# Kernel tuning notes

Measured on AMD Instinct MI355X. Metric: run time of the kernel, lower is better.

## Reference

```python
import jax, jax.numpy as jnp
import numpy as np

B, N1, N2 = 4, 16384, 4096   # scenes, fine points/scene, coarse points/scene
CIN, COUT = 512, 256
K = 3
EPS_BN = 1e-5
EPS_D = 1e-8


def setup_inputs() -> dict:
    key = jax.random.key(0)
    ks = jax.random.split(key, 6)
    return {
        "point_1": jax.random.uniform(ks[0], (B * N1, 3), dtype=jnp.float32),
        "feat_1": jax.random.normal(ks[1], (B * N1, COUT), dtype=jnp.float32) * 0.1,
        "point_2": jax.random.uniform(ks[2], (B * N2, 3), dtype=jnp.float32),
        "feat_2": jax.random.normal(ks[3], (B * N2, CIN), dtype=jnp.float32) * 0.1,
        "W1": jax.random.normal(ks[4], (COUT, COUT), dtype=jnp.float32) / np.sqrt(COUT).astype(np.float32),
        "b1": jnp.zeros((COUT,), jnp.float32),
        "g1": jnp.ones((COUT,), jnp.float32),
        "beta1": jnp.zeros((COUT,), jnp.float32),
        "W2": jax.random.normal(ks[5], (CIN, COUT), dtype=jnp.float32) / np.sqrt(CIN).astype(np.float32),
        "b2": jnp.zeros((COUT,), jnp.float32),
        "g2": jnp.ones((COUT,), jnp.float32),
        "beta2": jnp.zeros((COUT,), jnp.float32),
        # equal-sized segments: row_splits = [0, N, 2N, ...]
        "row_splits_1": jnp.arange(B + 1, dtype=jnp.int32) * N1,
        "row_splits_2": jnp.arange(B + 1, dtype=jnp.int32) * N2,
    }


def _bn(x, gamma, beta):
    # BatchNorm1d, training mode (biased variance, as in torch)
    mu = x.mean(0)
    var = x.var(0)
    return gamma * (x - mu) * jax.lax.rsqrt(var + EPS_BN) + beta


def reference(point_1, feat_1, point_2, feat_2,
              W1, b1, g1, beta1, W2, b2, g2, beta2,
              row_splits_1, row_splits_2):
    # linear1(feat_1): Linear + BN + ReLU
    f1 = jax.nn.relu(_bn(feat_1 @ W1 + b1, g1, beta1))          # [B*N1, COUT]
    # linear2(feat_2): Linear + BN + ReLU
    f2 = jax.nn.relu(_bn(feat_2 @ W2 + b2, g2, beta2))          # [B*N2, COUT]

    # batched KNN (equal row_splits -> reshape into [B, n, 3])
    q = point_1.reshape(B, N1, 3)
    p = point_2.reshape(B, N2, 3)
    d2 = ((q * q).sum(-1)[:, :, None]
          + (p * p).sum(-1)[:, None, :]
          - 2.0 * jnp.einsum("bnd,bmd->bnm", q, p))             # [B, N1, N2] squared dists
    neg_d, idx = jax.lax.top_k(-d2, K)                           # [B, N1, K]
    dist = jnp.maximum(-neg_d, 0.0)

    # inverse-distance weights (knn search is non-differentiable in the original)
    recip = 1.0 / (dist + EPS_D)
    w = jax.lax.stop_gradient(recip / recip.sum(-1, keepdims=True))  # [B, N1, K]

    # gather + weighted sum (three-interpolate)
    f2b = f2.reshape(B, N2, COUT)
    gathered = f2b[jnp.arange(B)[:, None, None], idx]            # [B, N1, K, COUT]
    interp = (gathered * w[..., None]).sum(2).reshape(B * N1, COUT)

    return f1 + interp
```

## Files before the change

### kernel.cpp

```cpp
#include <hip/hip_runtime.h>
#include <hip/hip_bf16.h>
#include <math.h>

#define N1R 65536
#define N2R 16384
#define NPB 4096
#define NQB 16384
#define CC  256
#define ASTRIDE 40
#define NCELL 512
#define GRID_FAIL_R2 0.015625f

typedef __attribute__((ext_vector_type(4))) float v4f;
typedef __attribute__((ext_vector_type(8))) short v8s;

static __device__ __forceinline__ short f2bs(float f) {
    union { __hip_bfloat16 h; short s; } u;
    u.h = __float2bfloat16(f);
    return u.s;
}

static __device__ __forceinline__ int cell_of(float x, float y, float z) {
    const int cx = min(7, (int)(x * 8.0f));
    const int cy = min(7, (int)(y * 8.0f));
    const int cz = min(7, (int)(z * 8.0f));
    return (cz << 6) | (cy << 3) | cx;
}

static __device__ __forceinline__ void ins3(float d, int si,
    float& b0, float& b1, float& b2, int& i0, int& i1, int& i2)
{
    const bool lt0 = (d < b0) | ((d == b0) & (si < i0));
    const bool lt1 = (d < b1) | ((d == b1) & (si < i1));
    const bool lt2 = (d < b2) | ((d == b2) & (si < i2));
    b2 = lt1 ? b1 : (lt2 ? d : b2);   i2 = lt1 ? i1 : (lt2 ? si : i2);
    b1 = lt0 ? b0 : (lt1 ? d : b1);   i1 = lt0 ? i0 : (lt1 ? si : i1);
    b0 = lt0 ? d  : b0;               i0 = lt0 ? si : i0;
}

__global__ __launch_bounds__(256)
void wtrans_kernel(const float* __restrict__ W, short* __restrict__ WT, int Kd)
{
    const int i = blockIdx.x * 256 + threadIdx.x;
    const int k = i >> 8;
    const int n = i & 255;
    WT[(size_t)n * Kd + k] = f2bs(W[i]);
}

__global__ __launch_bounds__(256)
void paug_count_kernel(const float* __restrict__ p2, float4* __restrict__ paug,
                       int* __restrict__ counts_p)
{
#pragma clang fp contract(off)
    const int i = blockIdx.x * 256 + threadIdx.x;
    const float x = p2[(size_t)i * 3 + 0];
    const float y = p2[(size_t)i * 3 + 1];
    const float z = p2[(size_t)i * 3 + 2];
    float4 v;
    v.x = x; v.y = y; v.z = z;
    v.w = (x * x + y * y) + z * z;
    paug[i] = v;
    const int b = i >> 12;
    atomicAdd(&counts_p[b * NCELL + cell_of(x, y, z)], 1);
}

__global__ __launch_bounds__(256)
void qcount_kernel(const float* __restrict__ p1, int* __restrict__ counts_q)
{
    const int i = blockIdx.x * 256 + threadIdx.x;
    const float x = p1[(size_t)i * 3 + 0];
    const float y = p1[(size_t)i * 3 + 1];
    const float z = p1[(size_t)i * 3 + 2];
    const int b = i >> 14;
    atomicAdd(&counts_q[b * NCELL + cell_of(x, y, z)], 1);
}

__global__ __launch_bounds__(512)
void prefix_kernel(const int* __restrict__ counts_p, int* __restrict__ cursors_p,
                   int* __restrict__ starts_p,
                   const int* __restrict__ counts_q, int* __restrict__ cursors_q)
{
    __shared__ int sc[512];
    const int t = threadIdx.x;
    for (int a = 0; a < 8; ++a) {
        const int b = a & 3;
        const int* cnt = (a < 4) ? counts_p + b * NCELL : counts_q + b * NCELL;
        const int v = cnt[t];
        sc[t] = v;
        __syncthreads();
        for (int off = 1; off < 512; off <<= 1) {
            const int add = (t >= off) ? sc[t - off] : 0;
            __syncthreads();
            sc[t] += add;
            __syncthreads();
        }
        const int incl = sc[t];
        const int excl = incl - v;
        if (a < 4) {
            starts_p[b * 513 + t] = excl;
            if (t == 511) starts_p[b * 513 + 512] = incl;
            cursors_p[b * NCELL + t] = excl;
        } else {
            cursors_q[b * NCELL + t] = excl;
        }
        __syncthreads();
    }
}

__global__ __launch_bounds__(256)
void scatter_p_kernel(const float4* __restrict__ paug, int* __restrict__ cursors,
                      float4* __restrict__ sortedP, unsigned short* __restrict__ sIdx)
{
    const int i = blockIdx.x * 256 + threadIdx.x;
    const float4 v = paug[i];
    const int b = i >> 12;
    const int cell = cell_of(v.x, v.y, v.z);
    const int pos = atomicAdd(&cursors[b * NCELL + cell], 1);
    sortedP[(size_t)b * NPB + pos] = v;
    sIdx[(size_t)b * NPB + pos] = (unsigned short)(i & 4095);
}

__global__ __launch_bounds__(256)
void scatter_q_kernel(const float* __restrict__ p1, int* __restrict__ cursors,
                      unsigned short* __restrict__ qlist)
{
    const int i = blockIdx.x * 256 + threadIdx.x;
    const float x = p1[(size_t)i * 3 + 0];
    const float y = p1[(size_t)i * 3 + 1];
    const float z = p1[(size_t)i * 3 + 2];
    const int b = i >> 14;
    const int cell = cell_of(x, y, z);
    const int pos = atomicAdd(&cursors[b * NCELL + cell], 1);
    qlist[(size_t)b * NQB + pos] = (unsigned short)(i & 16383);
}

__global__ __launch_bounds__(256)
void gemm_fused_kernel(const float* __restrict__ X,
                       const short* __restrict__ WT,
                       const float* __restrict__ bias,
                       float* __restrict__ Y,
                       float* __restrict__ partS, float* __restrict__ partQ,
                       int Kdim)
{
    __shared__ short As[128 * ASTRIDE];

    const int bm0 = blockIdx.x * 128;
    const int bn0 = blockIdx.y * 128;
    const int wave = threadIdx.x >> 6;
    const int lane = threadIdx.x & 63;
    const int wm0 = (wave >> 1) * 64;
    const int wn0 = (wave & 1) * 64;
    const int col = lane & 15, quad = lane >> 4;

    const int srow = threadIdx.x >> 1;
    const int skh  = (threadIdx.x & 1) * 16;
    const float* sbase = X + (size_t)(bm0 + srow) * Kdim + skh;
    short* sdst = As + srow * ASTRIDE + skh;

    v4f acc[4][4];
#pragma unroll
    for (int i = 0; i < 4; ++i)
#pragma unroll
        for (int j = 0; j < 4; ++j) acc[i][j] = (v4f){0.f, 0.f, 0.f, 0.f};

    const short* wbase = WT + (size_t)(bn0 + wn0 + col) * Kdim + quad * 8;

    v4f f0 = *(const v4f*)(sbase);
    v4f f1 = *(const v4f*)(sbase + 4);
    v4f f2v = *(const v4f*)(sbase + 8);
    v4f f3 = *(const v4f*)(sbase + 12);

    for (int k0 = 0; k0 < Kdim; k0 += 32) {
        v8s lo, hi;
#pragma unroll
        for (int j = 0; j < 4; ++j) {
            lo[j] = f2bs(f0[j]); lo[j + 4] = f2bs(f1[j]);
            hi[j] = f2bs(f2v[j]); hi[j + 4] = f2bs(f3[j]);
        }
        __syncthreads();
        *(v8s*)sdst = lo;
        *(v8s*)(sdst + 8) = hi;
        __syncthreads();

        v8s bf[4];
#pragma unroll
        for (int ni = 0; ni < 4; ++ni)
            bf[ni] = *(const v8s*)(wbase + (size_t)(ni * 16) * Kdim + k0);

        if (k0 + 32 < Kdim) {
            const float* np = sbase + k0 + 32;
            f0 = *(const v4f*)np;
            f1 = *(const v4f*)(np + 4);
            f2v = *(const v4f*)(np + 8);
            f3 = *(const v4f*)(np + 12);
        }

        v8s a[4];
#pragma unroll
        for (int mi = 0; mi < 4; ++mi)
            a[mi] = *(const v8s*)(As + (wm0 + mi * 16 + col) * ASTRIDE + quad * 8);
#pragma unroll
        for (int mi = 0; mi < 4; ++mi)
#pragma unroll
            for (int ni = 0; ni < 4; ++ni)
                acc[mi][ni] = __builtin_amdgcn_mfma_f32_16x16x32_bf16(a[mi], bf[ni], acc[mi][ni], 0, 0, 0);
    }

    float* pS = partS + (size_t)(blockIdx.x * 2 + (wave >> 1)) * CC;
    float* pQ = partQ + (size_t)(blockIdx.x * 2 + (wave >> 1)) * CC;
#pragma unroll
    for (int ni = 0; ni < 4; ++ni) {
        const int n = bn0 + wn0 + ni * 16 + col;
        const float bv = bias[n];
        float s = 0.f, q = 0.f;
#pragma unroll
        for (int mi = 0; mi < 4; ++mi) {
            const int m = bm0 + wm0 + mi * 16 + quad * 4;
#pragma unroll
            for (int r = 0; r < 4; ++r) {
                const float y = acc[mi][ni][r] + bv;
                Y[(size_t)(m + r) * CC + n] = y;
                s += y; q += y * y;
            }
        }
        s += __shfl_xor(s, 16); q += __shfl_xor(q, 16);
        s += __shfl_xor(s, 32); q += __shfl_xor(q, 32);
        if (quad == 0) { pS[n] = s; pQ[n] = q; }
    }
}

__global__ __launch_bounds__(256)
void stat_reduce_kernel(const float* __restrict__ pS1, const float* __restrict__ pQ1,
                        const float* __restrict__ pS2, const float* __restrict__ pQ2,
                        float* __restrict__ stats)
{
    const int c = threadIdx.x;
    const bool two = blockIdx.x >= 16;
    const float* pS = two ? pS2 : pS1;
    const float* pQ = two ? pQ2 : pQ1;
    const int r0 = (two ? (blockIdx.x - 16) : blockIdx.x) * 64;
    float s = 0.f, q = 0.f;
    for (int r = r0; r < r0 + 64; ++r) {
        s += pS[(size_t)r * CC + c];
        q += pQ[(size_t)r * CC + c];
    }
    float* st = stats + (two ? 512 : 0);
    atomicAdd(&st[c], s);
    atomicAdd(&st[256 + c], q);
}

__global__ __launch_bounds__(512)
void finalize_kernel(const float* __restrict__ sums,
                     const float* __restrict__ g1, const float* __restrict__ be1,
                     const float* __restrict__ g2, const float* __restrict__ be2,
                     float* __restrict__ ac)
{
    const int t = threadIdx.x;
    const int c = t & 255;
    const int which = t >> 8;
    const float* s = sums + which * 512;
    const double n = which ? (double)N2R : (double)N1R;
    const double mu = (double)s[c] / n;
    const double var = (double)s[c + 256] / n - mu * mu;
    const float g  = which ? g2[c]  : g1[c];
    const float be = which ? be2[c] : be1[c];
    const double a  = (double)g / sqrt(var + 1e-5);
    const double cv = (double)be - a * mu;
    ac[which * 512 + c]       = (float)a;
    ac[which * 512 + 256 + c] = (float)cv;
}

__global__ __launch_bounds__(256)
void knn_grid_kernel(const float* __restrict__ p1,
                     const float4* __restrict__ sortedP,
                     const unsigned short* __restrict__ sIdx16,
                     const int* __restrict__ starts_p,
                     const unsigned short* __restrict__ qlist,
                     int* __restrict__ idx_out, float* __restrict__ w_out,
                     int* __restrict__ failCount, int* __restrict__ failList)
{
#pragma clang fp contract(off)
    __shared__ float4 sP[NPB];
    __shared__ unsigned short sI[NPB];
    __shared__ int sS[513];
    __shared__ float mD[128 * 3];
    __shared__ int   mI[128 * 3];

    const int b = blockIdx.x >> 7;
    const int slot0 = (blockIdx.x & 127) * 128;
    const int tid = threadIdx.x;
    const int lq = tid & 127;
    const int half = tid >> 7;

    {
        const float4* gp = sortedP + (size_t)b * NPB;
        for (int i = tid; i < NPB; i += 256) sP[i] = gp[i];
        const unsigned int* gi = (const unsigned int*)(sIdx16 + (size_t)b * NPB);
        unsigned int* li = (unsigned int*)sI;
        for (int i = tid; i < NPB / 2; i += 256) li[i] = gi[i];
        const int* gs = starts_p + b * 513;
        for (int i = tid; i < 513; i += 256) sS[i] = gs[i];
    }

    const int q = qlist[(size_t)b * NQB + slot0 + lq];
    const int qid = b * NQB + q;
    const float qx = p1[(size_t)qid * 3 + 0];
    const float qy = p1[(size_t)qid * 3 + 1];
    const float qz = p1[(size_t)qid * 3 + 2];
    const float qq = (qx * qx + qy * qy) + qz * qz;
    const int cqx = min(7, (int)(qx * 8.0f));
    const int cqy = min(7, (int)(qy * 8.0f));
    const int cqz = min(7, (int)(qz * 8.0f));

    __syncthreads();

    float b0 = 3.0e38f, b1 = 3.0e38f, b2 = 3.0e38f;
    int i0 = 0x7fffffff, i1 = 0x7fffffff, i2 = 0x7fffffff;

    int n = 0;
    for (int dz = -1; dz <= 1; ++dz)
        for (int dy = -1; dy <= 1; ++dy)
            for (int dx = -1; dx <= 1; ++dx, ++n) {
                if (half ? (n < 14) : (n >= 14)) continue;
                const int cz = cqz + dz, cy = cqy + dy, cx = cqx + dx;
                if (((unsigned)cz | (unsigned)cy | (unsigned)cx) > 7u) continue;
                const int cell = (cz << 6) | (cy << 3) | cx;
                const int ks = sS[cell], ke = sS[cell + 1];
                for (int k = ks; k < ke; ++k) {
                    const float4 P = sP[k];
                    const int si = sI[k];
                    const float dot = fmaf(qz, P.z, fmaf(qy, P.y, qx * P.x));
                    const float d = fmaf(-2.0f, dot, qq + P.w);
                    ins3(d, si, b0, b1, b2, i0, i1, i2);
                }
            }

    if (half) {
        mD[lq * 3 + 0] = b0; mD[lq * 3 + 1] = b1; mD[lq * 3 + 2] = b2;
        mI[lq * 3 + 0] = i0; mI[lq * 3 + 1] = i1; mI[lq * 3 + 2] = i2;
    }
    __syncthreads();
    if (!half) {
#pragma unroll
        for (int r = 0; r < 3; ++r)
            ins3(mD[lq * 3 + r], mI[lq * 3 + r], b0, b1, b2, i0, i1, i2);

        if (!(b2 < GRID_FAIL_R2)) {
            const int p = atomicAdd(failCount, 1);
            if (p < N1R) failList[p] = qid;
        }
        const float r0 = 1.0f / (fmaxf(b0, 0.0f) + 1e-8f);
        const float r1 = 1.0f / (fmaxf(b1, 0.0f) + 1e-8f);
        const float r2 = 1.0f / (fmaxf(b2, 0.0f) + 1e-8f);
        const float rs = (r0 + r1) + r2;
        idx_out[(size_t)qid * 3 + 0] = i0;
        idx_out[(size_t)qid * 3 + 1] = i1;
        idx_out[(size_t)qid * 3 + 2] = i2;
        w_out[(size_t)qid * 3 + 0] = r0 / rs;
        w_out[(size_t)qid * 3 + 1] = r1 / rs;
        w_out[(size_t)qid * 3 + 2] = r2 / rs;
    }
}

__global__ __launch_bounds__(256)
void knn_bf_kernel(const float* __restrict__ p1,
                   const float4* __restrict__ paug,
                   const int* __restrict__ failCount,
                   const int* __restrict__ failList,
                   int* __restrict__ idx_out, float* __restrict__ w_out)
{
#pragma clang fp contract(off)
    const int nf = min(*failCount, N1R);
    const int gw = (blockIdx.x * 256 + threadIdx.x) >> 6;
    const int lane = threadIdx.x & 63;
    const int nw = (gridDim.x * 256) >> 6;

    for (int fi = gw; fi < nf; fi += nw) {
        const int qid = failList[fi];
        const int b = qid >> 14;
        const float qx = p1[(size_t)qid * 3 + 0];
        const float qy = p1[(size_t)qid * 3 + 1];
        const float qz = p1[(size_t)qid * 3 + 2];
        const float qq = (qx * qx + qy * qy) + qz * qz;

        float b0 = 3.0e38f, b1 = 3.0e38f, b2 = 3.0e38f;
        int i0 = 0x7fffffff, i1 = 0x7fffffff, i2 = 0x7fffffff;

        const float4* pb = paug + (size_t)b * NPB;
        for (int j = lane; j < NPB; j += 64) {
            const float4 P = pb[j];
            const float dot = fmaf(qz, P.z, fmaf(qy, P.y, qx * P.x));
            const float d = fmaf(-2.0f, dot, qq + P.w);
            ins3(d, j, b0, b1, b2, i0, i1, i2);
        }
        for (int m = 1; m < 64; m <<= 1) {
            const float c0 = __shfl_xor(b0, m), c1 = __shfl_xor(b1, m), c2 = __shfl_xor(b2, m);
            const int j0 = __shfl_xor(i0, m), j1 = __shfl_xor(i1, m), j2 = __shfl_xor(i2, m);
            ins3(c0, j0, b0, b1, b2, i0, i1, i2);
            ins3(c1, j1, b0, b1, b2, i0, i1, i2);
            ins3(c2, j2, b0, b1, b2, i0, i1, i2);
        }
        if (lane == 0) {
            const float r0 = 1.0f / (fmaxf(b0, 0.0f) + 1e-8f);
            const float r1 = 1.0f / (fmaxf(b1, 0.0f) + 1e-8f);
            const float r2 = 1.0f / (fmaxf(b2, 0.0f) + 1e-8f);
            const float rs = (r0 + r1) + r2;
            idx_out[(size_t)qid * 3 + 0] = i0;
            idx_out[(size_t)qid * 3 + 1] = i1;
            idx_out[(size_t)qid * 3 + 2] = i2;
            w_out[(size_t)qid * 3 + 0] = r0 / rs;
            w_out[(size_t)qid * 3 + 1] = r1 / rs;
            w_out[(size_t)qid * 3 + 2] = r2 / rs;
        }
    }
}

__global__ __launch_bounds__(256)
void final_kernel(float* __restrict__ Y1out,
                  const float* __restrict__ Y2raw,
                  const float* __restrict__ ac,
                  const int* __restrict__ idx, const float* __restrict__ w)
{
    const int r = blockIdx.x * 4 + (threadIdx.x >> 6);
    const int cg = threadIdx.x & 63;
    const int b = r >> 14;

    v4f a1 = *(const v4f*)(ac + cg * 4);
    v4f c1 = *(const v4f*)(ac + 256 + cg * 4);
    v4f a2 = *(const v4f*)(ac + 512 + cg * 4);
    v4f c2 = *(const v4f*)(ac + 768 + cg * 4);
    v4f y = *(const v4f*)(Y1out + (size_t)r * CC + cg * 4);
    v4f s;
#pragma unroll
    for (int j = 0; j < 4; ++j)
        s[j] = fmaxf(fmaf(a1[j], y[j], c1[j]), 0.f);

    const int*   ir = idx + (size_t)r * 3;
    const float* wr = w   + (size_t)r * 3;
#pragma unroll
    for (int k = 0; k < 3; ++k) {
        const int id = ir[k];
        const float wk = wr[k];
        v4f g = *(const v4f*)(Y2raw + ((size_t)(b * NPB + id)) * CC + cg * 4);
#pragma unroll
        for (int j = 0; j < 4; ++j) {
            const float gv = fmaxf(fmaf(a2[j], g[j], c2[j]), 0.f);
            s[j] = fmaf(wk, gv, s[j]);
        }
    }
    *(v4f*)(Y1out + (size_t)r * CC + cg * 4) = s;
}

extern "C" void kernel_launch(void* const* d_in, const int* in_sizes, int n_in,
                              void* d_out, int out_size, void* d_ws, size_t ws_size,
                              hipStream_t stream)
{
    const float* point1 = (const float*)d_in[0];
    const float* feat1  = (const float*)d_in[1];
    const float* point2 = (const float*)d_in[2];
    const float* feat2  = (const float*)d_in[3];
    const float* W1     = (const float*)d_in[4];
    const float* b1     = (const float*)d_in[5];
    const float* g1     = (const float*)d_in[6];
    const float* beta1  = (const float*)d_in[7];
    const float* W2     = (const float*)d_in[8];
    const float* b2     = (const float*)d_in[9];
    const float* g2     = (const float*)d_in[10];
    const float* beta2  = (const float*)d_in[11];

    float* Y1 = (float*)d_out;

    char* ws = (char*)d_ws;
    float*          Y2       = (float*)ws;
    float*          stats    = (float*)(ws + (size_t)16777216);
    int*            counts_p = (int*)  (ws + (size_t)16781312);
    int*            counts_q = (int*)  (ws + (size_t)16789504);
    int*            failCnt  = (int*)  (ws + (size_t)16797696);
    int*            cursors_p= (int*)  (ws + (size_t)16801792);
    int*            cursors_q= (int*)  (ws + (size_t)16809984);
    int*            starts_p = (int*)  (ws + (size_t)16818176);
    float*          ac       = (float*)(ws + (size_t)16826624);
    unsigned short* sIdx16   = (unsigned short*)(ws + (size_t)16830720);
    unsigned short* qlist    = (unsigned short*)(ws + (size_t)16863488);
    int*            failList = (int*)  (ws + (size_t)16994560);
    float4*         sortedP  = (float4*)(ws + (size_t)17256704);
    int*            idxb     = (int*)  (ws + (size_t)17518848);
    float*          wb       = (float*)(ws + (size_t)18305280);
    short*          WT1      = (short*)(ws + (size_t)19091712);
    short*          WT2      = (short*)(ws + (size_t)19222784);
    float4*         paug     = (float4*)(ws + (size_t)19484928);
    float*          partS1   = (float*)(ws + (size_t)19747072);
    float*          partQ1   = (float*)(ws + (size_t)20795648);
    float*          partS2   = (float*)(ws + (size_t)21844224);
    float*          partQ2   = (float*)(ws + (size_t)22106368);

    hipMemsetAsync(stats, 0, 24576, stream);

    wtrans_kernel<<<256, 256, 0, stream>>>(W1, WT1, 256);
    wtrans_kernel<<<512, 256, 0, stream>>>(W2, WT2, 512);

    paug_count_kernel<<<N2R / 256, 256, 0, stream>>>(point2, paug, counts_p);
    qcount_kernel<<<N1R / 256, 256, 0, stream>>>(point1, counts_q);
    prefix_kernel<<<1, 512, 0, stream>>>(counts_p, cursors_p, starts_p, counts_q, cursors_q);
    scatter_p_kernel<<<N2R / 256, 256, 0, stream>>>(paug, cursors_p, sortedP, sIdx16);
    scatter_q_kernel<<<N1R / 256, 256, 0, stream>>>(point1, cursors_q, qlist);

    gemm_fused_kernel<<<dim3(N1R / 128, 2), 256, 0, stream>>>(feat1, WT1, b1, Y1,
                                                              partS1, partQ1, 256);
    gemm_fused_kernel<<<dim3(N2R / 128, 2), 256, 0, stream>>>(feat2, WT2, b2, Y2,
                                                              partS2, partQ2, 512);

    stat_reduce_kernel<<<20, 256, 0, stream>>>(partS1, partQ1, partS2, partQ2, stats);
    finalize_kernel<<<1, 512, 0, stream>>>(stats, g1, beta1, g2, beta2, ac);

    knn_grid_kernel<<<512, 256, 0, stream>>>(point1, sortedP, sIdx16, starts_p,
                                             qlist, idxb, wb, failCnt, failList);
    knn_bf_kernel<<<256, 256, 0, stream>>>(point1, paug, failCnt, failList, idxb, wb);

    final_kernel<<<N1R / 4, 256, 0, stream>>>(Y1, Y2, ac, idxb, wb);
}
```

Baseline: 319.8 us.

## Merge small prep kernels, double-buffer GEMM LDS, template tile height, cell-ordered final pass

Merges the two weight-transpose kernels, the two histogram kernels and the two scatter kernels into single launches to cut launch overhead. The GEMM is templated on block rows with double-buffered LDS and a two-stage register prefetch, which removes one barrier per k-step; the second GEMM uses 64-row tiles for more blocks. The final kernel walks rows in spatial-cell order through qlist for better locality in gathers of Y2. Partial-stat buffers and the reduce grid are resized to match the extra GEMM blocks, which risks layout mistakes.

```diff
diff --git a/kernel.cpp b/kernel.cpp
--- a/kernel.cpp
+++ b/kernel.cpp
@@ -39,40 +39,45 @@
 }
 
 __global__ __launch_bounds__(256)
-void wtrans_kernel(const float* __restrict__ W, short* __restrict__ WT, int Kd)
+void wtrans_all_kernel(const float* __restrict__ W1f, const float* __restrict__ W2f,
+                       short* __restrict__ WT1, short* __restrict__ WT2)
 {
     const int i = blockIdx.x * 256 + threadIdx.x;
-    const int k = i >> 8;
-    const int n = i & 255;
-    WT[(size_t)n * Kd + k] = f2bs(W[i]);
-}
-
-__global__ __launch_bounds__(256)
-void paug_count_kernel(const float* __restrict__ p2, float4* __restrict__ paug,
-                       int* __restrict__ counts_p)
+    if (i < 65536) {
+        const int k = i >> 8, n = i & 255;
+        WT1[(size_t)n * 256 + k] = f2bs(W1f[i]);
+    } else {
+        const int j = i - 65536;
+        const int k = j >> 8, n = j & 255;
+        WT2[(size_t)n * 512 + k] = f2bs(W2f[j]);
+    }
+}
+
+__global__ __launch_bounds__(256)
+void hist_kernel(const float* __restrict__ p2, const float* __restrict__ p1,
+                 float4* __restrict__ paug,
+                 int* __restrict__ counts_p, int* __restrict__ counts_q)
 {
 #pragma clang fp contract(off)
-    const int i = blockIdx.x * 256 + threadIdx.x;
-    const float x = p2[(size_t)i * 3 + 0];
-    const float y = p2[(size_t)i * 3 + 1];
-    const float z = p2[(size_t)i * 3 + 2];
-    float4 v;
-    v.x = x; v.y = y; v.z = z;
-    v.w = (x * x + y * y) + z * z;
-    paug[i] = v;
-    const int b = i >> 12;
-    atomicAdd(&counts_p[b * NCELL + cell_of(x, y, z)], 1);
-}
-
-__global__ __launch_bounds__(256)
-void qcount_kernel(const float* __restrict__ p1, int* __restrict__ counts_q)
-{
-    const int i = blockIdx.x * 256 + threadIdx.x;
-    const float x = p1[(size_t)i * 3 + 0];
-    const float y = p1[(size_t)i * 3 + 1];
-    const float z = p1[(size_t)i * 3 + 2];
-    const int b = i >> 14;
-    atomicAdd(&counts_q[b * NCELL + cell_of(x, y, z)], 1);
+    if (blockIdx.x < 64) {
+        const int i = blockIdx.x * 256 + threadIdx.x;
+        const float x = p2[(size_t)i * 3 + 0];
+        const float y = p2[(size_t)i * 3 + 1];
+        const float z = p2[(size_t)i * 3 + 2];
+        float4 v;
+        v.x = x; v.y = y; v.z = z;
+        v.w = (x * x + y * y) + z * z;
+        paug[i] = v;
+        const int b = i >> 12;
+        atomicAdd(&counts_p[b * NCELL + cell_of(x, y, z)], 1);
+    } else {
+        const int i = (blockIdx.x - 64) * 256 + threadIdx.x;
+        const float x = p1[(size_t)i * 3 + 0];
+        const float y = p1[(size_t)i * 3 + 1];
+        const float z = p1[(size_t)i * 3 + 2];
+        const int b = i >> 14;
+        atomicAdd(&counts_q[b * NCELL + cell_of(x, y, z)], 1);
+    }
 }
 
 __global__ __launch_bounds__(512)
@@ -108,32 +113,32 @@
 }
 
 __global__ __launch_bounds__(256)
-void scatter_p_kernel(const float4* __restrict__ paug, int* __restrict__ cursors,
-                      float4* __restrict__ sortedP, unsigned short* __restrict__ sIdx)
-{
-    const int i = blockIdx.x * 256 + threadIdx.x;
-    const float4 v = paug[i];
-    const int b = i >> 12;
-    const int cell = cell_of(v.x, v.y, v.z);
-    const int pos = atomicAdd(&cursors[b * NCELL + cell], 1);
-    sortedP[(size_t)b * NPB + pos] = v;
-    sIdx[(size_t)b * NPB + pos] = (unsigned short)(i & 4095);
-}
-
-__global__ __launch_bounds__(256)
-void scatter_q_kernel(const float* __restrict__ p1, int* __restrict__ cursors,
-                      unsigned short* __restrict__ qlist)
-{
-    const int i = blockIdx.x * 256 + threadIdx.x;
-    const float x = p1[(size_t)i * 3 + 0];
-    const float y = p1[(size_t)i * 3 + 1];
-    const float z = p1[(size_t)i * 3 + 2];
-    const int b = i >> 14;
-    const int cell = cell_of(x, y, z);
-    const int pos = atomicAdd(&cursors[b * NCELL + cell], 1);
-    qlist[(size_t)b * NQB + pos] = (unsigned short)(i & 16383);
-}
-
+void scatter_kernel(const float4* __restrict__ paug, const float* __restrict__ p1,
+                    int* __restrict__ cursors_p, int* __restrict__ cursors_q,
+                    float4* __restrict__ sortedP, unsigned short* __restrict__ sIdx,
+                    unsigned short* __restrict__ qlist)
+{
+    if (blockIdx.x < 64) {
+        const int i = blockIdx.x * 256 + threadIdx.x;
+        const float4 v = paug[i];
+        const int b = i >> 12;
+        const int cell = cell_of(v.x, v.y, v.z);
+        const int pos = atomicAdd(&cursors_p[b * NCELL + cell], 1);
+        sortedP[(size_t)b * NPB + pos] = v;
+        sIdx[(size_t)b * NPB + pos] = (unsigned short)(i & 4095);
+    } else {
+        const int i = (blockIdx.x - 64) * 256 + threadIdx.x;
+        const float x = p1[(size_t)i * 3 + 0];
+        const float y = p1[(size_t)i * 3 + 1];
+        const float z = p1[(size_t)i * 3 + 2];
+        const int b = i >> 14;
+        const int cell = cell_of(x, y, z);
+        const int pos = atomicAdd(&cursors_q[b * NCELL + cell], 1);
+        qlist[(size_t)b * NQB + pos] = (unsigned short)(i & 16383);
+    }
+}
+
+template<int BM>
 __global__ __launch_bounds__(256)
 void gemm_fused_kernel(const float* __restrict__ X,
                        const short* __restrict__ WT,
@@ -142,65 +147,94 @@
                        float* __restrict__ partS, float* __restrict__ partQ,
                        int Kdim)
 {
-    __shared__ short As[128 * ASTRIDE];
-
-    const int bm0 = blockIdx.x * 128;
+    __shared__ short As[2][BM * ASTRIDE];
+
+    constexpr int MI  = BM / 32;
+    constexpr int NPF = BM / 32;
+    constexpr int TPR = 256 / BM;
+    constexpr int FPT = BM / 8;
+
+    const int bm0 = blockIdx.x * BM;
     const int bn0 = blockIdx.y * 128;
     const int wave = threadIdx.x >> 6;
     const int lane = threadIdx.x & 63;
-    const int wm0 = (wave >> 1) * 64;
+    const int wm0 = (wave >> 1) * (BM / 2);
     const int wn0 = (wave & 1) * 64;
     const int col = lane & 15, quad = lane >> 4;
 
-    const int srow = threadIdx.x >> 1;
-    const int skh  = (threadIdx.x & 1) * 16;
+    const int srow = threadIdx.x / TPR;
+    const int skh  = (threadIdx.x % TPR) * FPT;
     const float* sbase = X + (size_t)(bm0 + srow) * Kdim + skh;
-    short* sdst = As + srow * ASTRIDE + skh;
-
-    v4f acc[4][4];
-#pragma unroll
-    for (int i = 0; i < 4; ++i)
+    short* sdst0 = &As[0][srow * ASTRIDE + skh];
+    short* sdst1 = &As[1][srow * ASTRIDE + skh];
+
+    v4f acc[MI][4];
+#pragma unroll
+    for (int i = 0; i < MI; ++i)
 #pragma unroll
         for (int j = 0; j < 4; ++j) acc[i][j] = (v4f){0.f, 0.f, 0.f, 0.f};
 
     const short* wbase = WT + (size_t)(bn0 + wn0 + col) * Kdim + quad * 8;
 
-    v4f f0 = *(const v4f*)(sbase);
-    v4f f1 = *(const v4f*)(sbase + 4);
-    v4f f2v = *(const v4f*)(sbase + 8);
-    v4f f3 = *(const v4f*)(sbase + 12);
-
-    for (int k0 = 0; k0 < Kdim; k0 += 32) {
-        v8s lo, hi;
-#pragma unroll
-        for (int j = 0; j < 4; ++j) {
-            lo[j] = f2bs(f0[j]); lo[j + 4] = f2bs(f1[j]);
-            hi[j] = f2bs(f2v[j]); hi[j + 4] = f2bs(f3[j]);
+    v4f pf[NPF];
+#pragma unroll
+    for (int i = 0; i < NPF; ++i) pf[i] = *(const v4f*)(sbase + i * 4);
+    {
+        v8s wv;
+#pragma unroll
+        for (int j = 0; j < NPF / 2; ++j) {
+#pragma unroll
+            for (int t = 0; t < 4; ++t) {
+                wv[t]     = f2bs(pf[2 * j][t]);
+                wv[t + 4] = f2bs(pf[2 * j + 1][t]);
+            }
+            *(v8s*)(sdst0 + j * 8) = wv;
+        }
+    }
+    if (32 < Kdim)
+#pragma unroll
+        for (int i = 0; i < NPF; ++i) pf[i] = *(const v4f*)(sbase + 32 + i * 4);
+
+    const int NC = Kdim >> 5;
+    for (int c = 0; c < NC; ++c) {
+        const int k0 = c << 5;
+        const bool more = (c + 1 < NC);
+
+        v8s wv[NPF / 2];
+        if (more) {
+#pragma unroll
+            for (int j = 0; j < NPF / 2; ++j)
+#pragma unroll
+                for (int t = 0; t < 4; ++t) {
+                    wv[j][t]     = f2bs(pf[2 * j][t]);
+                    wv[j][t + 4] = f2bs(pf[2 * j + 1][t]);
+                }
         }
         __syncthreads();
-        *(v8s*)sdst = lo;
-        *(v8s*)(sdst + 8) = hi;
-        __syncthreads();
+        if (more) {
+            short* sd = (c & 1) ? sdst0 : sdst1;
+#pragma unroll
+            for (int j = 0; j < NPF / 2; ++j) *(v8s*)(sd + j * 8) = wv[j];
+        }
 
         v8s bf[4];
 #pragma unroll
         for (int ni = 0; ni < 4; ++ni)
             bf[ni] = *(const v8s*)(wbase + (size_t)(ni * 16) * Kdim + k0);
 
-        if (k0 + 32 < Kdim) {
-            const float* np = sbase + k0 + 32;
-            f0 = *(const v4f*)np;
-            f1 = *(const v4f*)(np + 4);
-            f2v = *(const v4f*)(np + 8);
-            f3 = *(const v4f*)(np + 12);
-        }
-
-        v8s a[4];
-#pragma unroll
-        for (int mi = 0; mi < 4; ++mi)
-            a[mi] = *(const v8s*)(As + (wm0 + mi * 16 + col) * ASTRIDE + quad * 8);
-#pragma unroll
-        for (int mi = 0; mi < 4; ++mi)
+        if (c + 2 < NC) {
+            const float* np = sbase + k0 + 64;
+#pragma unroll
+            for (int i = 0; i < NPF; ++i) pf[i] = *(const v4f*)(np + i * 4);
+        }
+
+        const short* bufc = As[c & 1];
+        v8s a[MI];
+#pragma unroll
+        for (int mi = 0; mi < MI; ++mi)
+            a[mi] = *(const v8s*)(bufc + (wm0 + mi * 16 + col) * ASTRIDE + quad * 8);
+#pragma unroll
+        for (int mi = 0; mi < MI; ++mi)
 #pragma unroll
             for (int ni = 0; ni < 4; ++ni)
                 acc[mi][ni] = __builtin_amdgcn_mfma_f32_16x16x32_bf16(a[mi], bf[ni], acc[mi][ni], 0, 0, 0);
@@ -214,7 +248,7 @@
         const float bv = bias[n];
         float s = 0.f, q = 0.f;
 #pragma unroll
-        for (int mi = 0; mi < 4; ++mi) {
+        for (int mi = 0; mi < MI; ++mi) {
             const int m = bm0 + wm0 + mi * 16 + quad * 4;
 #pragma unroll
             for (int r = 0; r < 4; ++r) {
@@ -419,11 +453,13 @@
 void final_kernel(float* __restrict__ Y1out,
                   const float* __restrict__ Y2raw,
                   const float* __restrict__ ac,
-                  const int* __restrict__ idx, const float* __restrict__ w)
-{
-    const int r = blockIdx.x * 4 + (threadIdx.x >> 6);
+                  const int* __restrict__ idx, const float* __restrict__ w,
+                  const unsigned short* __restrict__ qlist)
+{
+    const int slot = blockIdx.x * 4 + (threadIdx.x >> 6);
+    const int b = slot >> 14;
+    const int r = b * NQB + qlist[slot];
     const int cg = threadIdx.x & 63;
-    const int b = r >> 14;
 
     v4f a1 = *(const v4f*)(ac + cg * 4);
     v4f c1 = *(const v4f*)(ac + 256 + cg * 4);
@@ -492,30 +528,27 @@
     float*          partS1   = (float*)(ws + (size_t)19747072);
     float*          partQ1   = (float*)(ws + (size_t)20795648);
     float*          partS2   = (float*)(ws + (size_t)21844224);
-    float*          partQ2   = (float*)(ws + (size_t)22106368);
+    float*          partQ2   = (float*)(ws + (size_t)22368512);
 
     hipMemsetAsync(stats, 0, 24576, stream);
 
-    wtrans_kernel<<<256, 256, 0, stream>>>(W1, WT1, 256);
-    wtrans_kernel<<<512, 256, 0, stream>>>(W2, WT2, 512);
-
-    paug_count_kernel<<<N2R / 256, 256, 0, stream>>>(point2, paug, counts_p);
-    qcount_kernel<<<N1R / 256, 256, 0, stream>>>(point1, counts_q);
+    wtrans_all_kernel<<<768, 256, 0, stream>>>(W1, W2, WT1, WT2);
+    hist_kernel<<<320, 256, 0, stream>>>(point2, point1, paug, counts_p, counts_q);
     prefix_kernel<<<1, 512, 0, stream>>>(counts_p, cursors_p, starts_p, counts_q, cursors_q);
-    scatter_p_kernel<<<N2R / 256, 256, 0, stream>>>(paug, cursors_p, sortedP, sIdx16);
-    scatter_q_kernel<<<N1R / 256, 256, 0, stream>>>(point1, cursors_q, qlist);
-
-    gemm_fused_kernel<<<dim3(N1R / 128, 2), 256, 0, stream>>>(feat1, WT1, b1, Y1,
-                                                              partS1, partQ1, 256);
-    gemm_fused_kernel<<<dim3(N2R / 128, 2), 256, 0, stream>>>(feat2, WT2, b2, Y2,
-                                                              partS2, partQ2, 512);
-
-    stat_reduce_kernel<<<20, 256, 0, stream>>>(partS1, partQ1, partS2, partQ2, stats);
+    scatter_kernel<<<320, 256, 0, stream>>>(paug, point1, cursors_p, cursors_q,
+                                            sortedP, sIdx16, qlist);
+
+    gemm_fused_kernel<128><<<dim3(N1R / 128, 2), 256, 0, stream>>>(feat1, WT1, b1, Y1,
+                                                                   partS1, partQ1, 256);
+    gemm_fused_kernel<64><<<dim3(N2R / 64, 2), 256, 0, stream>>>(feat2, WT2, b2, Y2,
+                                                                 partS2, partQ2, 512);
+
+    stat_reduce_kernel<<<24, 256, 0, stream>>>(partS1, partQ1, partS2, partQ2, stats);
     finalize_kernel<<<1, 512, 0, stream>>>(stats, g1, beta1, g2, beta2, ac);
 
     knn_grid_kernel<<<512, 256, 0, stream>>>(point1, sortedP, sIdx16, starts_p,
                                              qlist, idxb, wb, failCnt, failList);
     knn_bf_kernel<<<256, 256, 0, stream>>>(point1, paug, failCnt, failList, idxb, wb);
 
-    final_kernel<<<N1R / 4, 256, 0, stream>>>(Y1, Y2, ac, idxb, wb);
-}
+    final_kernel<<<N1R / 4, 256, 0, stream>>>(Y1, Y2, ac, idxb, wb, qlist);
+}
```

New measurement: 315.4 us. About the same (-1.4%).
